# Optimization experiments

Measured on AMD Instinct MI355X. Metric: run time of the kernel, lower is better.

Reference implementation:

```python
import jax, jax.numpy as jnp
import numpy as np

V = 163842  # ico6 sphere vertex count
C_IN = 64
C_OUT = 64


def setup_inputs() -> dict:
    key = jax.random.key(0)
    k1, k2, k3, k4 = jax.random.split(key, 4)
    x = jax.random.normal(k1, (2, V, C_IN), dtype=jnp.float32)
    neigh_orders = jax.random.randint(k2, (V * 7,), 0, V, dtype=jnp.int64)
    W = jax.random.normal(k3, (C_OUT, 7 * C_IN), dtype=jnp.float32) * 0.05
    b = jax.random.normal(k4, (C_OUT,), dtype=jnp.float32) * 0.05
    return {"x": x, "neigh_orders": neigh_orders, "W": W, "b": b}


def reference(x, neigh_orders, W, b):
    B, Vn, C = x.shape
    # gather 7 neighbors per vertex: (B, V*7, C) -> (B, V, 7*C)
    mat = x[:, neigh_orders].reshape(B, Vn, 7 * C)
    # Linear: mat @ W.T + b -> (B, V, C_out)
    return jnp.einsum('bvk,ok->bvo', mat, W) + b
```

## Files before the change

### kernel.cpp

```cpp
#include <hip/hip_runtime.h>


constexpr int V_ICO   = 163842;
constexpr int M_TOTAL = 2 * V_ICO;
constexpr int X_ELEMS = M_TOTAL * 64;
constexpr int W_ELEMS = 64 * 448;
constexpr int XCH     = X_ELEMS / 8;
constexpr int WCH     = W_ELEMS / 8;

typedef __attribute__((ext_vector_type(4))) float          f32x4;
typedef __attribute__((ext_vector_type(4))) unsigned int   u32x4;
typedef __attribute__((ext_vector_type(8))) unsigned short u16x8;
typedef __attribute__((ext_vector_type(8))) __bf16         bf16x8;

union BF8 { u32x4 q; u16x8 u; bf16x8 v; };

static __device__ __forceinline__ unsigned short f2bf(float f) {
  unsigned int t = __float_as_uint(f);
  t += 0x7FFFu + ((t >> 16) & 1u);
  return (unsigned short)(t >> 16);
}

static __device__ __forceinline__ u32x4 cvt8(f32x4 a, f32x4 b) {
  BF8 r;
  r.u[0] = f2bf(a[0]); r.u[1] = f2bf(a[1]); r.u[2] = f2bf(a[2]); r.u[3] = f2bf(a[3]);
  r.u[4] = f2bf(b[0]); r.u[5] = f2bf(b[1]); r.u[6] = f2bf(b[2]); r.u[7] = f2bf(b[3]);
  return r.q;
}

__global__ __launch_bounds__(256)
void cvt_x_w(const float* __restrict__ x, const float* __restrict__ W,
             u32x4* __restrict__ xbf, u32x4* __restrict__ wbf) {
  const int i = blockIdx.x * blockDim.x + threadIdx.x;
  if (i >= XCH + WCH) return;
  const f32x4* src;
  u32x4* dst;
  if (i < XCH) {
    src = reinterpret_cast<const f32x4*>(x) + 2 * (size_t)i;
    dst = xbf + i;
  } else {
    const int k = i - XCH;
    src = reinterpret_cast<const f32x4*>(W) + 2 * (size_t)k;
    dst = wbf + k;
  }
  f32x4 f0 = src[0], f1 = src[1];
  __builtin_nontemporal_store(cvt8(f0, f1), dst);
}

__global__ __launch_bounds__(256)
void cvt_w_only(const float* __restrict__ W, u32x4* __restrict__ wbf) {
  const int i = blockIdx.x * blockDim.x + threadIdx.x;
  if (i < WCH) {
    const f32x4* src = reinterpret_cast<const f32x4*>(W) + 2 * (size_t)i;
    f32x4 f0 = src[0], f1 = src[1];
    wbf[i] = cvt8(f0, f1);
  }
}

template <int XBF, int WPRE>
__global__ __launch_bounds__(1024, 8)
void gather_mm(const float* __restrict__ x32, const unsigned short* __restrict__ x16,
               const int* __restrict__ neigh,
               const float* __restrict__ W32, const unsigned short* __restrict__ W16,
               const float* __restrict__ bias, float* __restrict__ out) {
  __shared__ __align__(16) unsigned short Wlds[64][456];

  const int tid = threadIdx.x;
  for (int i = tid; i < 64 * 56; i += 1024) {
    const int row = i / 56, ch = i - row * 56;
    u32x4 val;
    if constexpr (WPRE) {
      val = reinterpret_cast<const u32x4*>(W16)[i];
    } else {
      const f32x4* p = reinterpret_cast<const f32x4*>(W32 + row * 448 + ch * 8);
      val = cvt8(p[0], p[1]);
    }
    *reinterpret_cast<u32x4*>(&Wlds[row][ch * 8]) = val;
  }
  __syncthreads();

  const int w    = tid >> 6;
  const int lane = tid & 63;
  const int r    = lane & 15;
  const int g    = lane >> 4;
  const int m0   = blockIdx.x * 256 + w * 16;
  if (m0 >= M_TOTAL) return;

  int mA = m0 + r;
  if (mA > M_TOTAL - 1) mA = M_TOTAL - 1;
  const int bA = (mA >= V_ICO) ? 1 : 0;
  const int vA = mA - bA * V_ICO;

  int nofs[7];
#pragma unroll
  for (int j = 0; j < 7; ++j) nofs[j] = neigh[vA * 7 + j];

  const unsigned short* xb = nullptr;
  const float* xb32 = nullptr;
  if constexpr (XBF) xb   = x16 + (size_t)bA * V_ICO * 64 + (g << 3);
  else               xb32 = x32 + (size_t)bA * V_ICO * 64 + (g << 3);

  const unsigned short* wp = &Wlds[r][g << 3];

  const f32x4 zero = {0.f, 0.f, 0.f, 0.f};
  f32x4 acc0 = zero, acc1 = zero, acc2 = zero, acc3 = zero;

#define LOAD_J(d0, d1, j) do {                                              \
    if constexpr (XBF) {                                                    \
      const unsigned short* rp = xb + (size_t)nofs[j] * 64;                 \
      d0.q = *reinterpret_cast<const u32x4*>(rp);                           \
      d1.q = *reinterpret_cast<const u32x4*>(rp + 32);                      \
    } else {                                                                \
      const float* rp = xb32 + (size_t)nofs[j] * 64;                        \
      const f32x4* p0 = reinterpret_cast<const f32x4*>(rp);                 \
      const f32x4* p1 = reinterpret_cast<const f32x4*>(rp + 32);            \
      d0.q = cvt8(p0[0], p0[1]);                                            \
      d1.q = cvt8(p1[0], p1[1]);                                            \
    }                                                                       \
  } while (0)

#define MFMA_NT(afrag, nt, kc)                                              \
    acc##nt = __builtin_amdgcn_mfma_f32_16x16x32_bf16(                      \
        afrag.v,                                                            \
        *reinterpret_cast<const bf16x8*>(wp + (nt) * 16 * 456 + (kc) * 32), \
        acc##nt, 0, 0, 0)

#define COMPUTE_J(d0, d1, j) do {                                           \
    MFMA_NT(d0, 0, 2*(j));   MFMA_NT(d0, 1, 2*(j));                         \
    MFMA_NT(d0, 2, 2*(j));   MFMA_NT(d0, 3, 2*(j));                         \
    MFMA_NT(d1, 0, 2*(j)+1); MFMA_NT(d1, 1, 2*(j)+1);                       \
    MFMA_NT(d1, 2, 2*(j)+1); MFMA_NT(d1, 3, 2*(j)+1);                       \
  } while (0)

  BF8 a0lo, a0hi, a1lo, a1hi;
  LOAD_J(a0lo, a0hi, 0);
  LOAD_J(a1lo, a1hi, 1);
  COMPUTE_J(a0lo, a0hi, 0); LOAD_J(a0lo, a0hi, 2);
  COMPUTE_J(a1lo, a1hi, 1); LOAD_J(a1lo, a1hi, 3);
  COMPUTE_J(a0lo, a0hi, 2); LOAD_J(a0lo, a0hi, 4);
  COMPUTE_J(a1lo, a1hi, 3); LOAD_J(a1lo, a1hi, 5);
  COMPUTE_J(a0lo, a0hi, 4); LOAD_J(a0lo, a0hi, 6);
  COMPUTE_J(a1lo, a1hi, 5);
  COMPUTE_J(a0lo, a0hi, 6);

#undef LOAD_J
#undef MFMA_NT
#undef COMPUTE_J

  const float bv0 = bias[r], bv1 = bias[16 + r], bv2 = bias[32 + r], bv3 = bias[48 + r];
#pragma unroll
  for (int q2 = 0; q2 < 4; ++q2) {
    const int mS = m0 + (g << 2) + q2;
    if (mS < M_TOTAL) {
      float* o = out + (size_t)mS * 64;
      __builtin_nontemporal_store(acc0[q2] + bv0, o + r);
      __builtin_nontemporal_store(acc1[q2] + bv1, o + 16 + r);
      __builtin_nontemporal_store(acc2[q2] + bv2, o + 32 + r);
      __builtin_nontemporal_store(acc3[q2] + bv3, o + 48 + r);
    }
  }
}

extern "C" void kernel_launch(void* const* d_in, const int* in_sizes, int n_in,
                              void* d_out, int out_size, void* d_ws, size_t ws_size,
                              hipStream_t stream) {
  const float* x    = (const float*)d_in[0];
  const int*   nbr  = (const int*)d_in[1];
  const float* W    = (const float*)d_in[2];
  const float* bias = (const float*)d_in[3];
  float* out = (float*)d_out;

  const size_t xbf_bytes = (size_t)X_ELEMS * 2;
  const size_t wbf_bytes = (size_t)W_ELEMS * 2;
  const int grid_main = (M_TOTAL + 255) / 256;

  if (ws_size >= xbf_bytes + wbf_bytes) {
    u32x4* xbf = (u32x4*)d_ws;
    u32x4* wbf = (u32x4*)((char*)d_ws + xbf_bytes);
    hipLaunchKernelGGL(cvt_x_w, dim3((XCH + WCH + 255) / 256), dim3(256), 0, stream,
                       x, W, xbf, wbf);
    hipLaunchKernelGGL((gather_mm<1, 1>), dim3(grid_main), dim3(1024), 0, stream,
                       x, (const unsigned short*)xbf, nbr,
                       W, (const unsigned short*)wbf, bias, out);
  } else if (ws_size >= wbf_bytes) {
    u32x4* wbf = (u32x4*)d_ws;
    hipLaunchKernelGGL(cvt_w_only, dim3((WCH + 255) / 256), dim3(256), 0, stream, W, wbf);
    hipLaunchKernelGGL((gather_mm<0, 1>), dim3(grid_main), dim3(1024), 0, stream,
                       x, nullptr, nbr, W, (const unsigned short*)wbf, bias, out);
  } else {
    hipLaunchKernelGGL((gather_mm<0, 0>), dim3(grid_main), dim3(1024), 0, stream,
                       x, nullptr, nbr, W, nullptr, bias, out);
  }
}
```

Baseline: 207.6 us.

## Pre-swizzle W in LDS per MFMA fragment and deepen gather prefetch

Stores W in LDS in MFMA B-fragment order, so each lane reads a contiguous 16-byte chunk at lane*8 with no padding and no bank conflicts. Neighbor index loads are issued before the W staging so their latency overlaps the LDS fill. The bf16 path now keeps four neighbor rows in flight instead of two, and MFMA blocks are wrapped in s_setprio. The x conversion uses a normal store instead of a nontemporal one, which may keep the bf16 copy of x in cache for the following gather kernel. The cost is more registers per thread at 1024 threads per block.

```diff
diff --git a/kernel.cpp b/kernel.cpp
--- a/kernel.cpp
+++ b/kernel.cpp
@@ -44,7 +44,7 @@
     dst = wbf + k;
   }
   f32x4 f0 = src[0], f1 = src[1];
-  __builtin_nontemporal_store(cvt8(f0, f1), dst);
+  *dst = cvt8(f0, f1);
 }
 
 __global__ __launch_bounds__(256)
@@ -63,28 +63,14 @@
                const int* __restrict__ neigh,
                const float* __restrict__ W32, const unsigned short* __restrict__ W16,
                const float* __restrict__ bias, float* __restrict__ out) {
-  __shared__ __align__(16) unsigned short Wlds[64][456];
-
-  const int tid = threadIdx.x;
-  for (int i = tid; i < 64 * 56; i += 1024) {
-    const int row = i / 56, ch = i - row * 56;
-    u32x4 val;
-    if constexpr (WPRE) {
-      val = reinterpret_cast<const u32x4*>(W16)[i];
-    } else {
-      const f32x4* p = reinterpret_cast<const f32x4*>(W32 + row * 448 + ch * 8);
-      val = cvt8(p[0], p[1]);
-    }
-    *reinterpret_cast<u32x4*>(&Wlds[row][ch * 8]) = val;
-  }
-  __syncthreads();
-
+  __shared__ __align__(16) unsigned short Wlds[WCH * 8];
+
+  const int tid  = threadIdx.x;
   const int w    = tid >> 6;
   const int lane = tid & 63;
   const int r    = lane & 15;
   const int g    = lane >> 4;
   const int m0   = blockIdx.x * 256 + w * 16;
-  if (m0 >= M_TOTAL) return;
 
   int mA = m0 + r;
   if (mA > M_TOTAL - 1) mA = M_TOTAL - 1;
@@ -95,63 +81,90 @@
 #pragma unroll
   for (int j = 0; j < 7; ++j) nofs[j] = neigh[vA * 7 + j];
 
+  for (int i = tid; i < WCH; i += 1024) {
+    const int kcnt = i >> 6;
+    const int l    = i & 63;
+    const int row  = ((kcnt & 3) << 4) | (l & 15);
+    u32x4 val;
+    if constexpr (WPRE) {
+      const int c8 = ((kcnt >> 2) << 2) + (l >> 4);
+      val = reinterpret_cast<const u32x4*>(W16)[row * 56 + c8];
+    } else {
+      const int col = ((kcnt >> 2) << 5) + ((l >> 4) << 3);
+      const f32x4* p = reinterpret_cast<const f32x4*>(W32 + row * 448 + col);
+      val = cvt8(p[0], p[1]);
+    }
+    *reinterpret_cast<u32x4*>(&Wlds[(size_t)i * 8]) = val;
+  }
+  __syncthreads();
+  if (m0 >= M_TOTAL) return;
+
   const unsigned short* xb = nullptr;
   const float* xb32 = nullptr;
   if constexpr (XBF) xb   = x16 + (size_t)bA * V_ICO * 64 + (g << 3);
   else               xb32 = x32 + (size_t)bA * V_ICO * 64 + (g << 3);
 
-  const unsigned short* wp = &Wlds[r][g << 3];
+  const unsigned short* wp = Wlds + (lane << 3);
 
   const f32x4 zero = {0.f, 0.f, 0.f, 0.f};
   f32x4 acc0 = zero, acc1 = zero, acc2 = zero, acc3 = zero;
 
-#define LOAD_J(d0, d1, j) do {                                              \
-    if constexpr (XBF) {                                                    \
+#define MFMA_NT(af, nt, kc)                                                 \
+    acc##nt = __builtin_amdgcn_mfma_f32_16x16x32_bf16(                      \
+        af.v,                                                               \
+        *reinterpret_cast<const bf16x8*>(wp + ((kc) * 4 + (nt)) * 512),     \
+        acc##nt, 0, 0, 0)
+
+#define COMPUTE_J(dl, dh, j) do {                                           \
+    __builtin_amdgcn_s_setprio(1);                                          \
+    MFMA_NT(dl, 0, 2*(j));   MFMA_NT(dl, 1, 2*(j));                         \
+    MFMA_NT(dl, 2, 2*(j));   MFMA_NT(dl, 3, 2*(j));                         \
+    MFMA_NT(dh, 0, 2*(j)+1); MFMA_NT(dh, 1, 2*(j)+1);                       \
+    MFMA_NT(dh, 2, 2*(j)+1); MFMA_NT(dh, 3, 2*(j)+1);                       \
+    __builtin_amdgcn_s_setprio(0);                                          \
+  } while (0)
+
+  if constexpr (XBF) {
+#define LOAD_J(dl, dh, j) do {                                              \
       const unsigned short* rp = xb + (size_t)nofs[j] * 64;                 \
-      d0.q = *reinterpret_cast<const u32x4*>(rp);                           \
-      d1.q = *reinterpret_cast<const u32x4*>(rp + 32);                      \
-    } else {                                                                \
-      const float* rp = xb32 + (size_t)nofs[j] * 64;                        \
-      const f32x4* p0 = reinterpret_cast<const f32x4*>(rp);                 \
-      const f32x4* p1 = reinterpret_cast<const f32x4*>(rp + 32);            \
-      d0.q = cvt8(p0[0], p0[1]);                                            \
-      d1.q = cvt8(p1[0], p1[1]);                                            \
-    }                                                                       \
-  } while (0)
-
-#define MFMA_NT(afrag, nt, kc)                                              \
-    acc##nt = __builtin_amdgcn_mfma_f32_16x16x32_bf16(                      \
-        afrag.v,                                                            \
-        *reinterpret_cast<const bf16x8*>(wp + (nt) * 16 * 456 + (kc) * 32), \
-        acc##nt, 0, 0, 0)
-
-#define COMPUTE_J(d0, d1, j) do {                                           \
-    MFMA_NT(d0, 0, 2*(j));   MFMA_NT(d0, 1, 2*(j));                         \
-    MFMA_NT(d0, 2, 2*(j));   MFMA_NT(d0, 3, 2*(j));                         \
-    MFMA_NT(d1, 0, 2*(j)+1); MFMA_NT(d1, 1, 2*(j)+1);                       \
-    MFMA_NT(d1, 2, 2*(j)+1); MFMA_NT(d1, 3, 2*(j)+1);                       \
-  } while (0)
-
-  BF8 a0lo, a0hi, a1lo, a1hi;
-  LOAD_J(a0lo, a0hi, 0);
-  LOAD_J(a1lo, a1hi, 1);
-  COMPUTE_J(a0lo, a0hi, 0); LOAD_J(a0lo, a0hi, 2);
-  COMPUTE_J(a1lo, a1hi, 1); LOAD_J(a1lo, a1hi, 3);
-  COMPUTE_J(a0lo, a0hi, 2); LOAD_J(a0lo, a0hi, 4);
-  COMPUTE_J(a1lo, a1hi, 3); LOAD_J(a1lo, a1hi, 5);
-  COMPUTE_J(a0lo, a0hi, 4); LOAD_J(a0lo, a0hi, 6);
-  COMPUTE_J(a1lo, a1hi, 5);
-  COMPUTE_J(a0lo, a0hi, 6);
-
+      dl.q = *reinterpret_cast<const u32x4*>(rp);                           \
+      dh.q = *reinterpret_cast<const u32x4*>(rp + 32);                      \
+    } while (0)
+
+    BF8 b0l, b0h, b1l, b1h, b2l, b2h, b3l, b3h;
+    LOAD_J(b0l, b0h, 0);
+    LOAD_J(b1l, b1h, 1);
+    LOAD_J(b2l, b2h, 2);
+    LOAD_J(b3l, b3h, 3);
+    COMPUTE_J(b0l, b0h, 0); LOAD_J(b0l, b0h, 4);
+    COMPUTE_J(b1l, b1h, 1); LOAD_J(b1l, b1h, 5);
+    COMPUTE_J(b2l, b2h, 2); LOAD_J(b2l, b2h, 6);
+    COMPUTE_J(b3l, b3h, 3);
+    COMPUTE_J(b0l, b0h, 4);
+    COMPUTE_J(b1l, b1h, 5);
+    COMPUTE_J(b2l, b2h, 6);
 #undef LOAD_J
+  } else {
+#pragma unroll
+    for (int j = 0; j < 7; ++j) {
+      const float* rp = xb32 + (size_t)nofs[j] * 64;
+      const f32x4* p0 = reinterpret_cast<const f32x4*>(rp);
+      const f32x4* p1 = reinterpret_cast<const f32x4*>(rp + 32);
+      BF8 dl, dh;
+      dl.q = cvt8(p0[0], p0[1]);
+      dh.q = cvt8(p1[0], p1[1]);
+      COMPUTE_J(dl, dh, j);
+    }
+  }
 #undef MFMA_NT
 #undef COMPUTE_J
 
   const float bv0 = bias[r], bv1 = bias[16 + r], bv2 = bias[32 + r], bv3 = bias[48 + r];
+  const bool full = (m0 + 16 <= M_TOTAL);
 #pragma unroll
   for (int q2 = 0; q2 < 4; ++q2) {
     const int mS = m0 + (g << 2) + q2;
-    if (mS < M_TOTAL) {
+    if (full || mS < M_TOTAL) {
       float* o = out + (size_t)mS * 64;
       __builtin_nontemporal_store(acc0[q2] + bv0, o + r);
       __builtin_nontemporal_store(acc1[q2] + bv1, o + 16 + r);
```

Measured after the change: 201.5 us. -2.9%, faster.
